# Kernel tuning notes

Hardware: AMD Instinct MI355X
Metric: run time of the kernel (lower is better)

The kernel has to match this reference:

```python
import jax, jax.numpy as jnp
import numpy as np

B, S, DIM = 4, 2048, 512
HEADS, DHEAD = 8, 64
INNER = HEADS * DHEAD


def setup_inputs() -> dict:
    key = jax.random.key(0)
    k1, k2, k3, k4 = jax.random.split(key, 4)
    x = jax.random.normal(k1, (B, S, DIM), dtype=jnp.float32)
    W_qkv = jax.random.normal(k2, (DIM, 3 * INNER), dtype=jnp.float32) * (DIM ** -0.5)
    W_out = jax.random.normal(k3, (INNER, DIM), dtype=jnp.float32) * (INNER ** -0.5)
    b_out = jnp.zeros((DIM,), dtype=jnp.float32)
    # learnable log-temperature, initialized to log(dim_head**-0.5)
    log_temp = jnp.asarray(np.log(DHEAD ** -0.5), dtype=jnp.float32)
    return {"x": x, "W_qkv": W_qkv, "log_temp": log_temp, "W_out": W_out, "b_out": b_out}


def reference(x, W_qkv, log_temp, W_out, b_out):
    b, s, _ = x.shape
    qkv = x @ W_qkv  # [b, s, 3*inner]
    q, k, v = jnp.split(qkv, 3, axis=-1)
    # [b, s, inner] -> [b, h, s, d]
    reshape = lambda t: t.reshape(b, s, HEADS, DHEAD).transpose(0, 2, 1, 3)
    q, k, v = reshape(q), reshape(k), reshape(v)
    dots = jnp.einsum("bhid,bhjd->bhij", q, k) * jnp.exp(log_temp)
    mask_value = -jnp.finfo(dots.dtype).max
    eye = jnp.eye(s, dtype=bool)
    dots = jnp.where(eye, mask_value, dots)
    attn = jax.nn.softmax(dots, axis=-1)
    out = jnp.einsum("bhij,bhjd->bhid", attn, v)
    out = out.transpose(0, 2, 1, 3).reshape(b, s, INNER)
    return out @ W_out + b_out
```

## Files before the change

### kernel.cpp

```cpp
#include <hip/hip_runtime.h>
#include <hip/hip_bf16.h>

#define BB 4
#define SS 2048
#define DIMM 512
#define HH 8
#define DD 64
#define NQKV 1536

typedef float  floatx4 __attribute__((ext_vector_type(4)));
typedef short  bf16x8  __attribute__((ext_vector_type(8)));

#define MFMA16(A, B, C) __builtin_amdgcn_mfma_f32_16x16x32_bf16(A, B, C, 0, 0, 0)

__device__ __forceinline__ unsigned short f2bf(float f) {
    unsigned int u = __float_as_uint(f);
    u += 0x7FFFu + ((u >> 16) & 1u);
    return (unsigned short)(u >> 16);
}

__device__ __forceinline__ unsigned int f2bf_pk(float lo, float hi) {
    float2 f; f.x = lo; f.y = hi;
    __hip_bfloat162 h = __float22bfloat162_rn(f);
    return *reinterpret_cast<unsigned int*>(&h);
}

__device__ __forceinline__ float fast_exp2(float x) {
#if __has_builtin(__builtin_amdgcn_exp2f)
    return __builtin_amdgcn_exp2f(x);
#else
    return __exp2f(x);
#endif
}

__device__ __forceinline__ void gl_lds16(const void* g, void* l) {
    __builtin_amdgcn_global_load_lds(
        (__attribute__((address_space(1))) void*)g,
        (__attribute__((address_space(3))) void*)l,
        16, 0, 0);
}

__global__ __launch_bounds__(256) void k_cvt_x(const float* __restrict__ x,
                                               unsigned short* __restrict__ xb) {
    int i = (blockIdx.x * 256 + threadIdx.x) * 4;
    float4 v = *(const float4*)(x + i);
    ushort4 o;
    o.x = f2bf(v.x); o.y = f2bf(v.y); o.z = f2bf(v.z); o.w = f2bf(v.w);
    *(ushort4*)(xb + i) = o;
}

__global__ __launch_bounds__(256) void k_tr_cvt(const float* __restrict__ in,
                                                unsigned short* __restrict__ out,
                                                int R, int C) {
    __shared__ float t[32][33];
    int c0 = blockIdx.x * 32, r0 = blockIdx.y * 32;
    int tx = threadIdx.x, ty = threadIdx.y;
    for (int i = 0; i < 4; i++) {
        int r = r0 + ty + i * 8;
        t[ty + i * 8][tx] = in[(size_t)r * C + c0 + tx];
    }
    __syncthreads();
    for (int i = 0; i < 4; i++) {
        int c = c0 + ty + i * 8;
        out[(size_t)c * R + r0 + tx] = f2bf(t[tx][ty + i * 8]);
    }
}

__global__ __launch_bounds__(256) void k_gemm_qkv(
    const unsigned short* __restrict__ A,
    const unsigned short* __restrict__ Bt,
    const float* __restrict__ log_temp,
    unsigned short* __restrict__ Qb,
    unsigned short* __restrict__ Kb,
    unsigned short* __restrict__ Vt) {
    __shared__ unsigned short smem[2][128 * 64];
    unsigned short* As = smem[0];
    unsigned short* Bs = smem[1];
    const int K = 512;
    int m0 = blockIdx.x * 128, n0 = blockIdx.y * 128;
    int tid = threadIdx.x;
    int w = tid >> 6, lane = tid & 63;
    int c = lane & 15, q4 = lane >> 4;
    int wm = w >> 1, wn = w & 1;
    float qscale = __expf(log_temp[0]) * 1.44269504f;

    floatx4 acc[4][4] = {};

    for (int k0 = 0; k0 < K; k0 += 64) {
        __syncthreads();
        for (int i = 0; i < 4; i++) {
            int cidx = w * 256 + i * 64 + lane;
            int row = cidx >> 3, cc = cidx & 7;
            int gcc = cc ^ (row & 7);
            gl_lds16(A + (size_t)(m0 + row) * K + k0 + gcc * 8,
                     As + (size_t)(w * 256 + i * 64) * 8);
            gl_lds16(Bt + (size_t)(n0 + row) * K + k0 + gcc * 8,
                     Bs + (size_t)(w * 256 + i * 64) * 8);
        }
        __syncthreads();
        bf16x8 aF[2][4], bF[2][4];
        for (int kh = 0; kh < 2; kh++)
            for (int mt = 0; mt < 4; mt++) {
                int row = wm * 64 + mt * 16 + c;
                aF[kh][mt] = *(const bf16x8*)&As[row * 64 + (((kh * 4 + q4) ^ (row & 7)) * 8)];
            }
        for (int kh = 0; kh < 2; kh++)
            for (int nt = 0; nt < 4; nt++) {
                int row = wn * 64 + nt * 16 + c;
                bF[kh][nt] = *(const bf16x8*)&Bs[row * 64 + (((kh * 4 + q4) ^ (row & 7)) * 8)];
            }
        for (int kh = 0; kh < 2; kh++)
            for (int mt = 0; mt < 4; mt++)
                for (int nt = 0; nt < 4; nt++)
                    acc[mt][nt] = MFMA16(aF[kh][mt], bF[kh][nt], acc[mt][nt]);
    }

    if (n0 < 1024) {
        for (int nt = 0; nt < 4; nt++) {
            int n = n0 + wn * 64 + nt * 16 + c;
            int t = n >> 9, inner = n & 511;
            int h = inner >> 6, d = inner & 63;
            for (int mt = 0; mt < 4; mt++) {
                for (int r = 0; r < 4; r++) {
                    int m = m0 + wm * 64 + mt * 16 + q4 * 4 + r;
                    int b = m >> 11, s = m & 2047;
                    int bh = b * 8 + h;
                    float v = acc[mt][nt][r];
                    if (t == 0)  Qb[((size_t)bh * SS + s) * 64 + d] = f2bf(v * qscale);
                    else         Kb[((size_t)bh * SS + s) * 64 + d] = f2bf(v);
                }
            }
        }
    } else {
        unsigned short* T = &smem[0][0];
        int b = m0 >> 11, s_base = m0 & 2047;
        for (int half = 0; half < 2; half++) {
            __syncthreads();
            if (wn == half) {
                for (int nt = 0; nt < 4; nt++)
                    for (int mt = 0; mt < 4; mt++)
                        for (int r = 0; r < 4; r++)
                            T[(nt * 16 + c) * 136 + wm * 64 + mt * 16 + q4 * 4 + r] =
                                f2bf(acc[mt][nt][r]);
            }
            __syncthreads();
            for (int rr = 0; rr < 4; rr++) {
                int nl = w * 16 + rr * 4 + q4;
                int ml = c * 8;
                bf16x8 v = *(const bf16x8*)&T[nl * 136 + ml];
                int n = n0 + half * 64 + nl;
                int h = (n >> 6) - 16, d = n & 63;
                int bh = b * 8 + h;
                *(bf16x8*)(Vt + ((size_t)bh * 64 + d) * SS + s_base + ml) = v;
            }
        }
    }
}

__global__ __launch_bounds__(512, 2) void k_attn(
    const unsigned short* __restrict__ Qb,
    const unsigned short* __restrict__ Kb,
    const unsigned short* __restrict__ Vt,
    unsigned short* __restrict__ AO) {
    __shared__ unsigned short Ks[2][64 * 64];
    __shared__ unsigned short Vs[2][64 * 64];
    __shared__ unsigned short Ps[8][16 * 64];
    int q0 = blockIdx.x * 256;
    int h = blockIdx.y, b = blockIdx.z;
    int bh = b * 8 + h;
    int tid = threadIdx.x, w = tid >> 6, lane = tid & 63;
    int c = lane & 15, q4 = lane >> 4;

    const unsigned short* Kbase = Kb + (size_t)bh * SS * 64;
    const unsigned short* Vbase = Vt + (size_t)bh * 64 * SS;

    bf16x8 qf[2][2];
    for (int m = 0; m < 2; m++) {
        const unsigned short* qp = Qb + ((size_t)bh * SS + q0 + w * 32 + m * 16 + c) * 64;
        qf[m][0] = *(const bf16x8*)(qp + q4 * 8);
        qf[m][1] = *(const bf16x8*)(qp + 32 + q4 * 8);
    }
    bf16x8 ones;
    {
        short o1 = (c == 0) ? (short)0x3F80 : (short)0;
        for (int j = 0; j < 8; j++) ones[j] = o1;
    }

    int gl = tid;
    int grow = gl >> 3, gcc = (gl & 7) ^ (grow & 7);
    const unsigned short* ksrc = Kbase + (size_t)grow * 64 + gcc * 8;
    const unsigned short* vsrc = Vbase + (size_t)grow * SS + gcc * 8;

    int mask_j0 = (q0 + w * 32) & ~63;
    floatx4 oacc[2][4] = {};
    floatx4 lacc[2] = {};

    gl_lds16(ksrc, Ks[0] + w * 512);
    gl_lds16(vsrc, Vs[0] + w * 512);

    for (int j0 = 0; j0 < SS; j0 += 64) {
        int buf = (j0 >> 6) & 1;
        __syncthreads();
        if (j0 + 64 < SS) {
            int jn = j0 + 64;
            gl_lds16(ksrc + (size_t)jn * 64, Ks[buf ^ 1] + w * 512);
            gl_lds16(vsrc + jn, Vs[buf ^ 1] + w * 512);
        }

        bf16x8 kf[2][4], vf[2][4];
        for (int kh = 0; kh < 2; kh++)
            for (int nt = 0; nt < 4; nt++) {
                int row = nt * 16 + c;
                int sw = ((kh * 4 + q4) ^ (row & 7)) * 8;
                kf[kh][nt] = *(const bf16x8*)&Ks[buf][row * 64 + sw];
                vf[kh][nt] = *(const bf16x8*)&Vs[buf][row * 64 + sw];
            }

        for (int m = 0; m < 2; m++) {
            floatx4 sa[4] = {};
            for (int kh = 0; kh < 2; kh++)
                for (int nt = 0; nt < 4; nt++)
                    sa[nt] = MFMA16(qf[m][kh], kf[kh][nt], sa[nt]);

            int rowbase = q0 + w * 32 + m * 16 + q4 * 4;
            if (j0 == mask_j0) {
                for (int nt = 0; nt < 4; nt++)
                    for (int r = 0; r < 4; r++)
                        if (j0 + nt * 16 + c == rowbase + r) sa[nt][r] = -1e30f;
            }

            for (int nt = 0; nt < 4; nt++) {
                int jj = nt * 16 + c;
                int swb = ((jj >> 3) ^ 7) & 7;
                (void)swb;
                for (int r = 0; r < 4; r += 2) {
                    unsigned int pk = f2bf_pk(fast_exp2(sa[nt][r]),
                                              fast_exp2(sa[nt][r + 1]));
                    int mm0 = q4 * 4 + r, mm1 = mm0 + 1;
                    Ps[w][mm0 * 64 + (((jj >> 3) ^ (mm0 & 7)) * 8) + (jj & 7)] =
                        (unsigned short)pk;
                    Ps[w][mm1 * 64 + (((jj >> 3) ^ (mm1 & 7)) * 8) + (jj & 7)] =
                        (unsigned short)(pk >> 16);
                }
            }

            bf16x8 pa0 = *(const bf16x8*)&Ps[w][c * 64 + ((q4 ^ (c & 7)) * 8)];
            bf16x8 pa1 = *(const bf16x8*)&Ps[w][c * 64 + (((4 + q4) ^ (c & 7)) * 8)];

            lacc[m] = MFMA16(pa0, ones, lacc[m]);
            lacc[m] = MFMA16(pa1, ones, lacc[m]);
            for (int dt = 0; dt < 4; dt++) {
                oacc[m][dt] = MFMA16(pa0, vf[0][dt], oacc[m][dt]);
                oacc[m][dt] = MFMA16(pa1, vf[1][dt], oacc[m][dt]);
            }
        }
    }

    for (int m = 0; m < 2; m++)
        for (int r = 0; r < 4; r++) {
            float l = __shfl(lacc[m][r], q4 << 4, 64);
            float inv = 1.0f / l;
            int s = q0 + w * 32 + m * 16 + q4 * 4 + r;
            for (int dt = 0; dt < 4; dt++)
                AO[((size_t)b * SS + s) * 512 + h * 64 + dt * 16 + c] =
                    f2bf(oacc[m][dt][r] * inv);
        }
}

__global__ __launch_bounds__(256) void k_gemm_out(
    const unsigned short* __restrict__ A,
    const unsigned short* __restrict__ Bt,
    const float* __restrict__ bias,
    float* __restrict__ out) {
    __shared__ unsigned short As[128 * 64];
    __shared__ unsigned short Bs[128 * 64];
    const int K = 512;
    int m0 = blockIdx.x * 128, n0 = blockIdx.y * 128;
    int tid = threadIdx.x;
    int w = tid >> 6, lane = tid & 63;
    int c = lane & 15, q4 = lane >> 4;
    int wm = w >> 1, wn = w & 1;

    floatx4 acc[4][4] = {};

    for (int k0 = 0; k0 < K; k0 += 64) {
        __syncthreads();
        for (int i = 0; i < 4; i++) {
            int cidx = w * 256 + i * 64 + lane;
            int row = cidx >> 3, cc = cidx & 7;
            int gcc = cc ^ (row & 7);
            gl_lds16(A + (size_t)(m0 + row) * K + k0 + gcc * 8,
                     As + (size_t)(w * 256 + i * 64) * 8);
            gl_lds16(Bt + (size_t)(n0 + row) * K + k0 + gcc * 8,
                     Bs + (size_t)(w * 256 + i * 64) * 8);
        }
        __syncthreads();
        bf16x8 aF[2][4], bF[2][4];
        for (int kh = 0; kh < 2; kh++)
            for (int mt = 0; mt < 4; mt++) {
                int row = wm * 64 + mt * 16 + c;
                aF[kh][mt] = *(const bf16x8*)&As[row * 64 + (((kh * 4 + q4) ^ (row & 7)) * 8)];
            }
        for (int kh = 0; kh < 2; kh++)
            for (int nt = 0; nt < 4; nt++) {
                int row = wn * 64 + nt * 16 + c;
                bF[kh][nt] = *(const bf16x8*)&Bs[row * 64 + (((kh * 4 + q4) ^ (row & 7)) * 8)];
            }
        for (int kh = 0; kh < 2; kh++)
            for (int mt = 0; mt < 4; mt++)
                for (int nt = 0; nt < 4; nt++)
                    acc[mt][nt] = MFMA16(aF[kh][mt], bF[kh][nt], acc[mt][nt]);
    }

    for (int nt = 0; nt < 4; nt++) {
        int n = n0 + wn * 64 + nt * 16 + c;
        float bv = bias[n];
        for (int mt = 0; mt < 4; mt++) {
            for (int r = 0; r < 4; r++) {
                int m = m0 + wm * 64 + mt * 16 + q4 * 4 + r;
                out[(size_t)m * 512 + n] = acc[mt][nt][r] + bv;
            }
        }
    }
}

extern "C" void kernel_launch(void* const* d_in, const int* in_sizes, int n_in,
                              void* d_out, int out_size, void* d_ws, size_t ws_size,
                              hipStream_t stream) {
    const float* x        = (const float*)d_in[0];
    const float* W_qkv    = (const float*)d_in[1];
    const float* log_temp = (const float*)d_in[2];
    const float* W_out    = (const float*)d_in[3];
    const float* b_out    = (const float*)d_in[4];
    float* out = (float*)d_out;

    char* ws = (char*)d_ws;
    unsigned short* xb   = (unsigned short*)(ws + 0);
    unsigned short* Wq_t = (unsigned short*)(ws + 8388608);
    unsigned short* Wo_t = (unsigned short*)(ws + 9961472);
    unsigned short* Qb   = (unsigned short*)(ws + 10485760);
    unsigned short* Kb   = (unsigned short*)(ws + 18874368);
    unsigned short* Vt   = (unsigned short*)(ws + 27262976);
    unsigned short* AO   = (unsigned short*)(ws + 35651584);

    k_cvt_x<<<4096, 256, 0, stream>>>(x, xb);
    k_tr_cvt<<<dim3(48, 16), dim3(32, 8), 0, stream>>>(W_qkv, Wq_t, 512, 1536);
    k_tr_cvt<<<dim3(16, 16), dim3(32, 8), 0, stream>>>(W_out, Wo_t, 512, 512);
    k_gemm_qkv<<<dim3(64, 12), 256, 0, stream>>>(xb, Wq_t, log_temp, Qb, Kb, Vt);
    k_attn<<<dim3(8, 8, 4), 512, 0, stream>>>(Qb, Kb, Vt, AO);
    k_gemm_out<<<dim3(64, 4), 256, 0, stream>>>(AO, Wo_t, b_out, out);
}
```

Baseline: 168.0 us.

## Keep attention probabilities in registers via transposed S and K16 MFMA for PV

The attention kernel now computes S transposed (K as the A operand), so each lane's exp results line up directly with the A-operand layout of a 16x16x16 bf16 MFMA for P·V. This removes the per-wave LDS round trip for P and the ones-vector MFMA used for row sums, which are replaced by register accumulation plus cross-lane shuffles. Blocks shrink to 256 threads covering 128 queries, giving twice as many blocks. The three prep kernels are merged into one launch. Risks are twice as many K16 MFMAs for PV and a row sum taken from fp32 values that do not match the bf16-rounded P used in the PV product.

```diff
diff --git a/kernel.cpp b/kernel.cpp
--- a/kernel.cpp
+++ b/kernel.cpp
@@ -10,8 +10,20 @@
 
 typedef float  floatx4 __attribute__((ext_vector_type(4)));
 typedef short  bf16x8  __attribute__((ext_vector_type(8)));
+typedef short  bf16x4  __attribute__((ext_vector_type(4)));
 
 #define MFMA16(A, B, C) __builtin_amdgcn_mfma_f32_16x16x32_bf16(A, B, C, 0, 0, 0)
+
+__device__ __forceinline__ floatx4 MFMA16K16(bf16x4 a, bf16x4 b, floatx4 c) {
+#if __has_builtin(__builtin_amdgcn_mfma_f32_16x16x16bf16_1k)
+    return __builtin_amdgcn_mfma_f32_16x16x16bf16_1k(a, b, c, 0, 0, 0);
+#else
+    floatx4 d;
+    asm volatile("v_mfma_f32_16x16x16_bf16 %0, %1, %2, %3"
+                 : "=v"(d) : "v"(a), "v"(b), "v"(c));
+    return d;
+#endif
+}
 
 __device__ __forceinline__ unsigned short f2bf(float f) {
     unsigned int u = __float_as_uint(f);
@@ -40,29 +52,34 @@
         16, 0, 0);
 }
 
-__global__ __launch_bounds__(256) void k_cvt_x(const float* __restrict__ x,
-                                               unsigned short* __restrict__ xb) {
-    int i = (blockIdx.x * 256 + threadIdx.x) * 4;
-    float4 v = *(const float4*)(x + i);
-    ushort4 o;
-    o.x = f2bf(v.x); o.y = f2bf(v.y); o.z = f2bf(v.z); o.w = f2bf(v.w);
-    *(ushort4*)(xb + i) = o;
-}
-
-__global__ __launch_bounds__(256) void k_tr_cvt(const float* __restrict__ in,
-                                                unsigned short* __restrict__ out,
-                                                int R, int C) {
+__global__ __launch_bounds__(256) void k_prep(
+    const float* __restrict__ x, const float* __restrict__ W_qkv,
+    const float* __restrict__ W_out,
+    unsigned short* __restrict__ xb, unsigned short* __restrict__ Wq_t,
+    unsigned short* __restrict__ Wo_t) {
     __shared__ float t[32][33];
-    int c0 = blockIdx.x * 32, r0 = blockIdx.y * 32;
-    int tx = threadIdx.x, ty = threadIdx.y;
+    int bid = blockIdx.x, tid = threadIdx.x;
+    if (bid < 4096) {
+        int i = (bid * 256 + tid) * 4;
+        float4 v = *(const float4*)(x + i);
+        ushort4 o;
+        o.x = f2bf(v.x); o.y = f2bf(v.y); o.z = f2bf(v.z); o.w = f2bf(v.w);
+        *(ushort4*)(xb + i) = o;
+        return;
+    }
+    const float* in; unsigned short* out; int R = 512, C, bx, by;
+    if (bid < 4864) { in = W_qkv; out = Wq_t; C = 1536; int blk = bid - 4096; bx = blk % 48; by = blk / 48; }
+    else            { in = W_out; out = Wo_t; C = 512;  int blk = bid - 4864; bx = blk % 16; by = blk / 16; }
+    int tx = tid & 31, ty = tid >> 5;
+    int c0 = bx * 32, r0 = by * 32;
     for (int i = 0; i < 4; i++) {
         int r = r0 + ty + i * 8;
         t[ty + i * 8][tx] = in[(size_t)r * C + c0 + tx];
     }
     __syncthreads();
     for (int i = 0; i < 4; i++) {
-        int c = c0 + ty + i * 8;
-        out[(size_t)c * R + r0 + tx] = f2bf(t[tx][ty + i * 8]);
+        int cc = c0 + ty + i * 8;
+        out[(size_t)cc * R + r0 + tx] = f2bf(t[tx][ty + i * 8]);
     }
 }
 
@@ -157,15 +174,14 @@
     }
 }
 
-__global__ __launch_bounds__(512, 2) void k_attn(
+__global__ __launch_bounds__(256, 4) void k_attn(
     const unsigned short* __restrict__ Qb,
     const unsigned short* __restrict__ Kb,
     const unsigned short* __restrict__ Vt,
     unsigned short* __restrict__ AO) {
     __shared__ unsigned short Ks[2][64 * 64];
     __shared__ unsigned short Vs[2][64 * 64];
-    __shared__ unsigned short Ps[8][16 * 64];
-    int q0 = blockIdx.x * 256;
+    int q0 = blockIdx.x * 128;
     int h = blockIdx.y, b = blockIdx.z;
     int bh = b * 8 + h;
     int tid = threadIdx.x, w = tid >> 6, lane = tid & 63;
@@ -175,96 +191,96 @@
     const unsigned short* Vbase = Vt + (size_t)bh * 64 * SS;
 
     bf16x8 qf[2][2];
-    for (int m = 0; m < 2; m++) {
-        const unsigned short* qp = Qb + ((size_t)bh * SS + q0 + w * 32 + m * 16 + c) * 64;
-        qf[m][0] = *(const bf16x8*)(qp + q4 * 8);
-        qf[m][1] = *(const bf16x8*)(qp + 32 + q4 * 8);
-    }
-    bf16x8 ones;
-    {
-        short o1 = (c == 0) ? (short)0x3F80 : (short)0;
-        for (int j = 0; j < 8; j++) ones[j] = o1;
-    }
-
-    int gl = tid;
-    int grow = gl >> 3, gcc = (gl & 7) ^ (grow & 7);
-    const unsigned short* ksrc = Kbase + (size_t)grow * 64 + gcc * 8;
-    const unsigned short* vsrc = Vbase + (size_t)grow * SS + gcc * 8;
+    for (int mi = 0; mi < 2; mi++) {
+        const unsigned short* qp = Qb + ((size_t)bh * SS + q0 + w * 32 + mi * 16 + c) * 64;
+        qf[mi][0] = *(const bf16x8*)(qp + q4 * 8);
+        qf[mi][1] = *(const bf16x8*)(qp + 32 + q4 * 8);
+    }
+
+    const unsigned short* ksrc[2];
+    const unsigned short* vsrc[2];
+    for (int i = 0; i < 2; i++) {
+        int cidx = i * 256 + tid;
+        int grow = cidx >> 3, gcc = (cidx & 7) ^ (grow & 7);
+        ksrc[i] = Kbase + (size_t)grow * 64 + gcc * 8;
+        vsrc[i] = Vbase + (size_t)grow * SS + gcc * 8;
+    }
+
+    for (int i = 0; i < 2; i++) {
+        gl_lds16(ksrc[i], Ks[0] + (i * 256 + w * 64) * 8);
+        gl_lds16(vsrc[i], Vs[0] + (i * 256 + w * 64) * 8);
+    }
 
     int mask_j0 = (q0 + w * 32) & ~63;
+    int mglob0 = q0 + w * 32 + c;
+    int mglob1 = mglob0 + 16;
     floatx4 oacc[2][4] = {};
-    floatx4 lacc[2] = {};
-
-    gl_lds16(ksrc, Ks[0] + w * 512);
-    gl_lds16(vsrc, Vs[0] + w * 512);
+    float psum0 = 0.f, psum1 = 0.f;
 
     for (int j0 = 0; j0 < SS; j0 += 64) {
         int buf = (j0 >> 6) & 1;
         __syncthreads();
         if (j0 + 64 < SS) {
-            int jn = j0 + 64;
-            gl_lds16(ksrc + (size_t)jn * 64, Ks[buf ^ 1] + w * 512);
-            gl_lds16(vsrc + jn, Vs[buf ^ 1] + w * 512);
-        }
-
-        bf16x8 kf[2][4], vf[2][4];
-        for (int kh = 0; kh < 2; kh++)
-            for (int nt = 0; nt < 4; nt++) {
-                int row = nt * 16 + c;
-                int sw = ((kh * 4 + q4) ^ (row & 7)) * 8;
-                kf[kh][nt] = *(const bf16x8*)&Ks[buf][row * 64 + sw];
-                vf[kh][nt] = *(const bf16x8*)&Vs[buf][row * 64 + sw];
-            }
-
-        for (int m = 0; m < 2; m++) {
-            floatx4 sa[4] = {};
-            for (int kh = 0; kh < 2; kh++)
-                for (int nt = 0; nt < 4; nt++)
-                    sa[nt] = MFMA16(qf[m][kh], kf[kh][nt], sa[nt]);
-
-            int rowbase = q0 + w * 32 + m * 16 + q4 * 4;
-            if (j0 == mask_j0) {
-                for (int nt = 0; nt < 4; nt++)
-                    for (int r = 0; r < 4; r++)
-                        if (j0 + nt * 16 + c == rowbase + r) sa[nt][r] = -1e30f;
-            }
-
-            for (int nt = 0; nt < 4; nt++) {
-                int jj = nt * 16 + c;
-                int swb = ((jj >> 3) ^ 7) & 7;
-                (void)swb;
-                for (int r = 0; r < 4; r += 2) {
-                    unsigned int pk = f2bf_pk(fast_exp2(sa[nt][r]),
-                                              fast_exp2(sa[nt][r + 1]));
-                    int mm0 = q4 * 4 + r, mm1 = mm0 + 1;
-                    Ps[w][mm0 * 64 + (((jj >> 3) ^ (mm0 & 7)) * 8) + (jj & 7)] =
-                        (unsigned short)pk;
-                    Ps[w][mm1 * 64 + (((jj >> 3) ^ (mm1 & 7)) * 8) + (jj & 7)] =
-                        (unsigned short)(pk >> 16);
+            for (int i = 0; i < 2; i++) {
+                gl_lds16(ksrc[i] + (size_t)(j0 + 64) * 64, Ks[buf ^ 1] + (i * 256 + w * 64) * 8);
+                gl_lds16(vsrc[i] + (j0 + 64), Vs[buf ^ 1] + (i * 256 + w * 64) * 8);
+            }
+        }
+        bool diag = (j0 == mask_j0);
+
+        for (int jt = 0; jt < 4; jt++) {
+            int row = jt * 16 + c;
+            bf16x8 kf0 = *(const bf16x8*)&Ks[buf][row * 64 + ((q4 ^ (row & 7)) * 8)];
+            bf16x8 kf1 = *(const bf16x8*)&Ks[buf][row * 64 + (((4 + q4) ^ (row & 7)) * 8)];
+            floatx4 sa0 = {}, sa1 = {};
+            sa0 = MFMA16(kf0, qf[0][0], sa0);
+            sa0 = MFMA16(kf1, qf[0][1], sa0);
+            sa1 = MFMA16(kf0, qf[1][0], sa1);
+            sa1 = MFMA16(kf1, qf[1][1], sa1);
+
+            if (diag) {
+                for (int r = 0; r < 4; r++) {
+                    int jg = j0 + jt * 16 + q4 * 4 + r;
+                    if (jg == mglob0) sa0[r] = -1e30f;
+                    if (jg == mglob1) sa1[r] = -1e30f;
                 }
             }
 
-            bf16x8 pa0 = *(const bf16x8*)&Ps[w][c * 64 + ((q4 ^ (c & 7)) * 8)];
-            bf16x8 pa1 = *(const bf16x8*)&Ps[w][c * 64 + (((4 + q4) ^ (c & 7)) * 8)];
-
-            lacc[m] = MFMA16(pa0, ones, lacc[m]);
-            lacc[m] = MFMA16(pa1, ones, lacc[m]);
+            float e0 = fast_exp2(sa0[0]), e1 = fast_exp2(sa0[1]);
+            float e2 = fast_exp2(sa0[2]), e3 = fast_exp2(sa0[3]);
+            psum0 += (e0 + e1) + (e2 + e3);
+            union { bf16x4 v; unsigned int u[2]; } P0;
+            P0.u[0] = f2bf_pk(e0, e1); P0.u[1] = f2bf_pk(e2, e3);
+            float f0 = fast_exp2(sa1[0]), f1 = fast_exp2(sa1[1]);
+            float f2 = fast_exp2(sa1[2]), f3 = fast_exp2(sa1[3]);
+            psum1 += (f0 + f1) + (f2 + f3);
+            union { bf16x4 v; unsigned int u[2]; } P1;
+            P1.u[0] = f2bf_pk(f0, f1); P1.u[1] = f2bf_pk(f2, f3);
+
+            int chunk = jt * 2 + (q4 >> 1);
+            int sub = (q4 & 1) * 4;
             for (int dt = 0; dt < 4; dt++) {
-                oacc[m][dt] = MFMA16(pa0, vf[0][dt], oacc[m][dt]);
-                oacc[m][dt] = MFMA16(pa1, vf[1][dt], oacc[m][dt]);
-            }
-        }
-    }
-
-    for (int m = 0; m < 2; m++)
+                int vrow = dt * 16 + c;
+                bf16x4 vf = *(const bf16x4*)&Vs[buf][vrow * 64 + ((chunk ^ (vrow & 7)) * 8) + sub];
+                oacc[0][dt] = MFMA16K16(P0.v, vf, oacc[0][dt]);
+                oacc[1][dt] = MFMA16K16(P1.v, vf, oacc[1][dt]);
+            }
+        }
+    }
+
+    for (int mi = 0; mi < 2; mi++) {
+        float l = (mi == 0) ? psum0 : psum1;
+        l += __shfl_xor(l, 16);
+        l += __shfl_xor(l, 32);
         for (int r = 0; r < 4; r++) {
-            float l = __shfl(lacc[m][r], q4 << 4, 64);
-            float inv = 1.0f / l;
-            int s = q0 + w * 32 + m * 16 + q4 * 4 + r;
+            float lr = __shfl(l, q4 * 4 + r, 64);
+            float inv = 1.0f / lr;
+            int s = q0 + w * 32 + mi * 16 + q4 * 4 + r;
             for (int dt = 0; dt < 4; dt++)
                 AO[((size_t)b * SS + s) * 512 + h * 64 + dt * 16 + c] =
-                    f2bf(oacc[m][dt][r] * inv);
-        }
+                    f2bf(oacc[mi][dt][r] * inv);
+        }
+    }
 }
 
 __global__ __launch_bounds__(256) void k_gemm_out(
@@ -343,10 +359,8 @@
     unsigned short* Vt   = (unsigned short*)(ws + 27262976);
     unsigned short* AO   = (unsigned short*)(ws + 35651584);
 
-    k_cvt_x<<<4096, 256, 0, stream>>>(x, xb);
-    k_tr_cvt<<<dim3(48, 16), dim3(32, 8), 0, stream>>>(W_qkv, Wq_t, 512, 1536);
-    k_tr_cvt<<<dim3(16, 16), dim3(32, 8), 0, stream>>>(W_out, Wo_t, 512, 512);
+    k_prep<<<5120, 256, 0, stream>>>(x, W_qkv, W_out, xb, Wq_t, Wo_t);
     k_gemm_qkv<<<dim3(64, 12), 256, 0, stream>>>(xb, Wq_t, log_temp, Qb, Kb, Vt);
-    k_attn<<<dim3(8, 8, 4), 512, 0, stream>>>(Qb, Kb, Vt, AO);
+    k_attn<<<dim3(16, 8, 4), 256, 0, stream>>>(Qb, Kb, Vt, AO);
     k_gemm_out<<<dim3(64, 4), 256, 0, stream>>>(AO, Wo_t, b_out, out);
 }
```

Measured after the change: 167.9 us. About the same (-0.0%).
